# Optimization experiments

Measured on AMD Instinct MI355X. Metric: run time of the kernel, lower is better.

The kernel has to match this reference:

```python
import jax, jax.numpy as jnp
import numpy as np

N = 256          # batch size
C = 100          # nb_classes
D = 512          # sz_embed
SCALE = 3.0
EPS = 1e-12      # F.normalize eps
M = N * (N - 1) // 2  # number of (i<j) candidate pairs


def l2norm(x):
    # matches F.normalize(p=2, dim=-1) with eps=1e-12
    return x / jnp.maximum(jnp.linalg.norm(x, axis=-1, keepdims=True), EPS)


def dist_block(A, B):
    # squared euclidean distance block of pairwise_distance(cat([A,B]))[0][:len(A), len(A):]
    # (off-diagonal block, so the eye-masking in the original is a no-op; negatives zeroed)
    d = (A * A).sum(-1, keepdims=True) + (B * B).sum(-1)[None, :] - 2.0 * (A @ B.T)
    return jnp.maximum(d, 0.0)


def setup_inputs() -> dict:
    key = jax.random.key(0)
    k1, k2, k3 = jax.random.split(key, 3)
    X = jax.random.normal(k1, (N, D), dtype=jnp.float32)
    proxies = jax.random.normal(k2, (C, D), dtype=jnp.float32) / 8.0
    T = jax.random.randint(k3, (N,), 0, C)
    indices = jnp.arange(N)  # unused by forward, kept for signature fidelity
    return {"X": X, "proxies": proxies, "T": T, "indices": indices}


def reference(X, proxies, T, indices):
    Pn = SCALE * l2norm(proxies)           # (C, D)
    Xn = SCALE * l2norm(X)                 # (N, D)
    IP = Xn @ Pn.T                         # (N, C) inner-product block

    # --- intercls_mixup (method=1, uncertainty-guided lambdas) ---
    # all i<j pairs; same-class pairs are masked out (original skips them in a Python loop)
    i1, i2 = jnp.triu_indices(N, k=1)      # (M,), (M,)
    diff = T[i1] != T[i2]                  # (M,) valid cross-class pairs
    c1, c2 = T[i1], T[i2]

    X1P1 = jnp.clip(IP[i1, c1], -1.0, 1.0)
    X1P2 = jnp.clip(IP[i1, c2], -1.0, 1.0)
    X2P1 = jnp.clip(IP[i2, c1], -1.0, 1.0)
    X2P2 = jnp.clip(IP[i2, c2], -1.0, 1.0)
    lam = jnp.clip((X2P2 - X2P1) / (X2P2 - X2P1 + X1P1 - X1P2), 0.3, 0.7)
    lam = jnp.where(diff, lam, 0.5)        # neutralize masked (same-class) pairs

    virt = lam[:, None] * Xn[i1] + (1.0 - lam[:, None]) * Xn[i2]  # (M, D)
    virt = l2norm(virt)

    # --- proxy-NCA loss over real + virtual samples ---
    Xall = jnp.concatenate([Xn, SCALE * virt], axis=0)            # (N+M, D)
    Dall = dist_block(Xall, Pn)                                   # (N+M, C)
    logsm = jax.nn.log_softmax(-Dall, axis=-1)

    loss_real = -logsm[jnp.arange(N), T]                          # one-hot targets
    lv = logsm[N:]                                                # (M, C)
    rows = jnp.arange(M)
    # virtual soft targets: lam*onehot(c1) + (1-lam)*onehot(c2)
    loss_virt = -(lam * lv[rows, c1] + (1.0 - lam) * lv[rows, c2])

    total = loss_real.sum() + jnp.sum(jnp.where(diff, loss_virt, 0.0))
    count = N + diff.sum()
    return total / count
```

## Files before the change

### kernel.cpp

```cpp
#include <hip/hip_runtime.h>
#include <hip/hip_bf16.h>
#include <math.h>

#define N_ 256
#define C_ 100
#define D_ 512
#define LOG2E 1.44269504088896f

#define WS_GX  0
#define WS_GTP 65536
#define WS_RN  91136

typedef __attribute__((ext_vector_type(8))) short short8;
typedef __attribute__((ext_vector_type(4))) float floatx4;

__device__ inline float waveReduceSum(float v) {
    #pragma unroll
    for (int off = 32; off > 0; off >>= 1) v += __shfl_xor(v, off, 64);
    return v;
}
__device__ inline float clip1(float x) { return fminf(fmaxf(x, -1.0f), 1.0f); }

__device__ inline short8 cvt8(float4 a, float4 b) {
    union { __hip_bfloat16 h[8]; short8 s; } u;
    u.h[0] = __float2bfloat16(a.x); u.h[1] = __float2bfloat16(a.y);
    u.h[2] = __float2bfloat16(a.z); u.h[3] = __float2bfloat16(a.w);
    u.h[4] = __float2bfloat16(b.x); u.h[5] = __float2bfloat16(b.y);
    u.h[6] = __float2bfloat16(b.z); u.h[7] = __float2bfloat16(b.w);
    return u.s;
}

__global__ __launch_bounds__(1024)
void gemm_kernel(const float* __restrict__ X, const float* __restrict__ P,
                 float* __restrict__ ws) {
    float* Gx  = ws + WS_GX;
    float* GTP = ws + WS_GTP;
    float* rn  = ws + WS_RN;
    __shared__ floatx4 accl[15][64];
    __shared__ float normp[16][16];
    int tile = blockIdx.x;
    int t = threadIdx.x, w = t >> 6, lane = t & 63;
    int r = lane & 15, quad = lane >> 4;
    const float *arow, *brow;
    int tm, tn, mode;
    if (tile < 136) {
        mode = 0;
        int u = tile; tm = 0;
        while (u >= 16 - tm) { u -= 16 - tm; ++tm; }
        tn = tm + u;
        arow = X + (size_t)(tm * 16 + r) * D_;
        brow = X + (size_t)(tn * 16 + r) * D_;
    } else {
        int u = tile - 136; mode = 1; tm = u / 7; tn = u - tm * 7;
        int pb = tn * 16 + r; if (pb >= C_) pb = 0;
        arow = X + (size_t)(tm * 16 + r) * D_;
        brow = P + (size_t)pb * D_;
    }
    int k0 = w * 32;
    const float4* ap = (const float4*)(arow + k0 + quad * 8);
    const float4* bp = (const float4*)(brow + k0 + quad * 8);
    float4 a0 = ap[0], a1v = ap[1];
    float4 b0 = bp[0], b1v = bp[1];
    short8 av = cvt8(a0, a1v);
    short8 bv = cvt8(b0, b1v);
    floatx4 acc = {0.0f, 0.0f, 0.0f, 0.0f};
    acc = __builtin_amdgcn_mfma_f32_16x16x32_bf16(av, bv, acc, 0, 0, 0);
    float s8 = b0.x*b0.x + b0.y*b0.y + b0.z*b0.z + b0.w*b0.w
             + b1v.x*b1v.x + b1v.y*b1v.y + b1v.z*b1v.z + b1v.w*b1v.w;
    s8 += __shfl_xor(s8, 16, 64);
    s8 += __shfl_xor(s8, 32, 64);
    if (quad == 0) normp[w][r] = s8;
    if (w) accl[w - 1][lane] = acc;
    __syncthreads();
    if (w == 0) {
        #pragma unroll
        for (int i = 0; i < 15; ++i) acc += accl[i][lane];
        int row0 = tm * 16 + quad * 4, col = tn * 16 + r;
        if (mode == 0) {
            #pragma unroll
            for (int i = 0; i < 4; ++i) Gx[(row0 + i) * 256 + col] = acc[i];
            if (tm == tn && (r >> 2) == quad)
                rn[tm * 16 + r] = 3.0f * rsqrtf(fmaxf(acc[r & 3], 1e-24f));
        } else {
            float cn = 0.0f;
            #pragma unroll
            for (int i = 0; i < 16; ++i) cn += normp[i][r];
            float spc = 3.0f * rsqrtf(fmaxf(cn, 1e-24f));
            int c = col;
            if (c < C_) {
                #pragma unroll
                for (int i = 0; i < 4; ++i)
                    GTP[(c >> 2) * 1024 + (row0 + i) * 4 + (c & 3)] = acc[i] * spc;
            }
        }
    }
}

__global__ __launch_bounds__(1024)
void pair_kernel(const float* __restrict__ ws, const int* __restrict__ T,
                 float* __restrict__ out) {
    const float* Gx   = ws + WS_GX;
    const float4* G4  = (const float4*)(ws + WS_GTP);
    const float* GTPf = ws + WS_GTP;
    const float* rn   = ws + WS_RN;
    __shared__ __attribute__((aligned(16))) float wbufA[16][104];
    __shared__ int hist[C_];
    __shared__ float red[16];

    int t = threadIdx.x, w = t >> 6, lane = t & 63;
    int b = blockIdx.x;
    int m = t >> 2, p = t & 3;

    int t1 = T[b];
    int t2 = T[m];
    float s1 = rn[b], sc2 = rn[m];
    float graw = 0.0f;
    if (m >= b) graw = Gx[b * 256 + m];
    float4 a2r[7];
    #pragma unroll
    for (int k = 0; k < 7; ++k) {
        int q = p + 4 * k;
        a2r[k] = (float4){0.f, 0.f, 0.f, 0.f};
        if (q < 25 && m >= b) a2r[k] = G4[q * 256 + m];
    }
    float u2t1 = GTPf[(t1 >> 2) * 1024 + m * 4 + (t1 & 3)];
    float u2t2 = GTPf[(t2 >> 2) * 1024 + m * 4 + (t2 & 3)];
    int Tt = (t < 256) ? T[t] : 0;
    if (t < C_) hist[t] = 0;
    if (lane < 25) {
        float4 av = G4[lane * 256 + b];
        *(float4*)&wbufA[w][lane * 4] = av;
    }

    bool diag = (m == b);
    bool act = diag || ((m > b) && (t2 != t1));
    float contrib = 0.0f;
    if (act) {
        float ip11 = wbufA[w][t1] * s1, ip12 = wbufA[w][t2] * s1;
        float ip21 = u2t1 * sc2,        ip22 = u2t2 * sc2;
        float X1P1 = clip1(ip11), X1P2 = clip1(ip12);
        float X2P1 = clip1(ip21), X2P2 = clip1(ip22);
        float num = X2P2 - X2P1;
        float den = num + X1P1 - X1P2;
        float lam = fminf(fmaxf(num / den, 0.3f), 0.7f);
        if (diag) lam = 1.0f;
        float oml = 1.0f - lam;
        float g = graw * s1 * sc2;
        float wn2 = 9.0f * (lam * lam + oml * oml) + 2.0f * lam * oml * g;
        float ss2 = 6.0f * rsqrtf(fmaxf(wn2, 1e-24f));
        float la = ss2 * lam * s1 * LOG2E, lb = ss2 * oml * sc2 * LOG2E;
        float sm0 = 0.0f, sm1 = 0.0f, sm2 = 0.0f, sm3 = 0.0f;
        #pragma unroll
        for (int k = 0; k < 7; ++k) {
            int q = p + 4 * k;
            if (q < 25) {
                float4 a1 = *(const float4*)&wbufA[w][q * 4];
                float4 a2 = a2r[k];
                sm0 += exp2f(la * a1.x + lb * a2.x);
                sm1 += exp2f(la * a1.y + lb * a2.y);
                sm2 += exp2f(la * a1.z + lb * a2.z);
                sm3 += exp2f(la * a1.w + lb * a2.w);
            }
        }
        float sm = (sm0 + sm1) + (sm2 + sm3);
        sm += __shfl_xor(sm, 1, 64);
        sm += __shfl_xor(sm, 2, 64);
        if (p == 0) {
            float LSE = logf(sm);
            float ec1 = ss2 * (lam * ip11 + oml * ip21);
            float ec2 = ss2 * (lam * ip12 + oml * ip22);
            contrib = LSE - lam * ec1 - oml * ec2;
        }
    }
    float rsum = waveReduceSum(contrib);
    if (lane == 0) red[w] = rsum;
    __syncthreads();
    if (t < 256) atomicAdd(&hist[Tt], 1);
    __syncthreads();
    if (w == 0) {
        float same;
        { float n = (float)hist[lane]; same = 0.5f * n * (n - 1.0f); }
        if (lane + 64 < C_) { float n = (float)hist[lane + 64]; same += 0.5f * n * (n - 1.0f); }
        float bs = (lane < 16) ? red[lane] : 0.0f;
        same = waveReduceSum(same);
        bs = waveReduceSum(bs);
        if (lane == 0) atomicAdd(out, bs / (32896.0f - same));
    }
}

extern "C" void kernel_launch(void* const* d_in, const int* in_sizes, int n_in,
                              void* d_out, int out_size, void* d_ws, size_t ws_size,
                              hipStream_t stream) {
    const float* X = (const float*)d_in[0];
    const float* P = (const float*)d_in[1];
    const int*   T = (const int*)d_in[2];
    float* ws = (float*)d_ws;
    float* out = (float*)d_out;

    gemm_kernel<<<248, 1024, 0, stream>>>(X, P, ws);
    pair_kernel<<<N_, 1024, 0, stream>>>(ws, T, out);
}
```

Before: 69.35 us.

## Balance pair kernel work with cyclic offset pairing and 8 threads per pair

Each pair_kernel block previously handled row b against columns m ≥ b, so the triangular workload gave block 0 far more active pairs than late blocks. Now each block handles a cyclic band of 128 offsets (b, b+d mod 256). The d = 128 half-band is taken only by blocks below 128, so every unordered pair is processed exactly once and per-block work is nearly uniform. Each pair now uses 8 lanes instead of 4, so the per-thread class loop drops from 7 to 4 steps, with one extra shuffle step in the reduction. The diagonal (real-sample) term becomes a second iteration for the first thread group, which makes that group slightly longer than the rest.

```diff
diff --git a/kernel.cpp b/kernel.cpp
--- a/kernel.cpp
+++ b/kernel.cpp
@@ -86,11 +86,10 @@
             #pragma unroll
             for (int i = 0; i < 16; ++i) cn += normp[i][r];
             float spc = 3.0f * rsqrtf(fmaxf(cn, 1e-24f));
-            int c = col;
-            if (c < C_) {
+            if (col < C_) {
                 #pragma unroll
                 for (int i = 0; i < 4; ++i)
-                    GTP[(c >> 2) * 1024 + (row0 + i) * 4 + (c & 3)] = acc[i] * spc;
+                    GTP[(col >> 2) * 1024 + (row0 + i) * 4 + (col & 3)] = acc[i] * spc;
             }
         }
     }
@@ -109,22 +108,29 @@
 
     int t = threadIdx.x, w = t >> 6, lane = t & 63;
     int b = blockIdx.x;
-    int m = t >> 2, p = t & 3;
-
+    int m = t >> 3, p = t & 7;
+
+    int d = m + 1;
+    int i2 = (b + d) & 255;
     int t1 = T[b];
-    int t2 = T[m];
-    float s1 = rn[b], sc2 = rn[m];
+    int t2 = T[i2];
+    float s1 = rn[b], sc2 = rn[i2];
+    bool pairact = (t2 != t1) && (d < 128 || b < 128);
+    int lo = min(b, i2), hi = max(b, i2);
     float graw = 0.0f;
-    if (m >= b) graw = Gx[b * 256 + m];
-    float4 a2r[7];
+    if (pairact) graw = Gx[lo * 256 + hi];
+    float4 a2r[4];
     #pragma unroll
-    for (int k = 0; k < 7; ++k) {
-        int q = p + 4 * k;
+    for (int k = 0; k < 4; ++k) {
+        int q = p + 8 * k;
         a2r[k] = (float4){0.f, 0.f, 0.f, 0.f};
-        if (q < 25 && m >= b) a2r[k] = G4[q * 256 + m];
-    }
-    float u2t1 = GTPf[(t1 >> 2) * 1024 + m * 4 + (t1 & 3)];
-    float u2t2 = GTPf[(t2 >> 2) * 1024 + m * 4 + (t2 & 3)];
+        if (q < 25 && pairact) a2r[k] = G4[q * 256 + i2];
+    }
+    float u2t1 = 0.0f, u2t2 = 0.0f;
+    if (pairact) {
+        u2t1 = GTPf[(t1 >> 2) * 1024 + i2 * 4 + (t1 & 3)];
+        u2t2 = GTPf[(t2 >> 2) * 1024 + i2 * 4 + (t2 & 3)];
+    }
     int Tt = (t < 256) ? T[t] : 0;
     if (t < C_) hist[t] = 0;
     if (lane < 25) {
@@ -132,44 +138,51 @@
         *(float4*)&wbufA[w][lane * 4] = av;
     }
 
-    bool diag = (m == b);
-    bool act = diag || ((m > b) && (t2 != t1));
     float contrib = 0.0f;
-    if (act) {
-        float ip11 = wbufA[w][t1] * s1, ip12 = wbufA[w][t2] * s1;
-        float ip21 = u2t1 * sc2,        ip22 = u2t2 * sc2;
+    int nit = (m == 0) ? 2 : 1;
+    for (int it = 0; it < nit; ++it) {
+        bool isdiag = (it == 1);
+        if (!(isdiag || pairact)) continue;
+        int t2v = isdiag ? t1 : t2;
+        float sc2v = isdiag ? s1 : sc2;
+        float ip11 = wbufA[w][t1] * s1;
+        float ip12 = wbufA[w][t2v] * s1;
+        float u2a = isdiag ? wbufA[w][t1] : u2t1;
+        float u2b = isdiag ? wbufA[w][t2v] : u2t2;
+        float ip21 = u2a * sc2v, ip22 = u2b * sc2v;
         float X1P1 = clip1(ip11), X1P2 = clip1(ip12);
         float X2P1 = clip1(ip21), X2P2 = clip1(ip22);
         float num = X2P2 - X2P1;
         float den = num + X1P1 - X1P2;
         float lam = fminf(fmaxf(num / den, 0.3f), 0.7f);
-        if (diag) lam = 1.0f;
+        if (isdiag) lam = 1.0f;
         float oml = 1.0f - lam;
-        float g = graw * s1 * sc2;
+        float g = graw * s1 * sc2v;
         float wn2 = 9.0f * (lam * lam + oml * oml) + 2.0f * lam * oml * g;
         float ss2 = 6.0f * rsqrtf(fmaxf(wn2, 1e-24f));
-        float la = ss2 * lam * s1 * LOG2E, lb = ss2 * oml * sc2 * LOG2E;
+        float la = ss2 * lam * s1 * LOG2E, lb = ss2 * oml * sc2v * LOG2E;
         float sm0 = 0.0f, sm1 = 0.0f, sm2 = 0.0f, sm3 = 0.0f;
         #pragma unroll
-        for (int k = 0; k < 7; ++k) {
-            int q = p + 4 * k;
+        for (int k = 0; k < 4; ++k) {
+            int q = p + 8 * k;
             if (q < 25) {
                 float4 a1 = *(const float4*)&wbufA[w][q * 4];
-                float4 a2 = a2r[k];
+                float4 a2 = isdiag ? a1 : a2r[k];
                 sm0 += exp2f(la * a1.x + lb * a2.x);
                 sm1 += exp2f(la * a1.y + lb * a2.y);
                 sm2 += exp2f(la * a1.z + lb * a2.z);
                 sm3 += exp2f(la * a1.w + lb * a2.w);
             }
         }
-        float sm = (sm0 + sm1) + (sm2 + sm3);
-        sm += __shfl_xor(sm, 1, 64);
-        sm += __shfl_xor(sm, 2, 64);
+        float smv = (sm0 + sm1) + (sm2 + sm3);
+        smv += __shfl_xor(smv, 1, 64);
+        smv += __shfl_xor(smv, 2, 64);
+        smv += __shfl_xor(smv, 4, 64);
         if (p == 0) {
-            float LSE = logf(sm);
+            float LSE = logf(smv);
             float ec1 = ss2 * (lam * ip11 + oml * ip21);
             float ec2 = ss2 * (lam * ip12 + oml * ip22);
-            contrib = LSE - lam * ec1 - oml * ec2;
+            contrib += LSE - lam * ec1 - oml * ec2;
         }
     }
     float rsum = waveReduceSum(contrib);
```

Measured after the change: 71.10 us. 2.5% more time.
